# Kernel optimization log

Measured on AMD Instinct MI355X. Metric: run time of the kernel, lower is better.

The kernel has to match this reference:

```python
import jax, jax.numpy as jnp
import numpy as np

B, L, D, H, HD, K = 1, 1024, 1024, 16, 64, 16
EPS = 1e-5

def _l2norm(x):
    n = jnp.sqrt(jnp.sum(x * x, axis=-1, keepdims=True))
    return x / jnp.maximum(n, 1e-12)

def _lin(x, w, b):
    return x @ w.T + b

def _lrelu2(x, alpha=0.01):
    y = jnp.where(x > 0, x, alpha * x)
    return y * y

def _forward(x, spectral_basis, M_phi_w, M_phi_b, wq_w, wq_b, wk_w, wk_b,
             wv_w, wv_b, wo_w, wo_b, wg_z_w, wg_z_b, kv_norm_scale):
    Bx, Lx, Dx = x.shape
    bhld = x.reshape(Bx, Lx, H, HD).transpose(0, 2, 1, 3)          # [B,H,L,h]
    # stu_conv: causal conv of every channel with each of K shared filters (FFT form)
    n = 2 * Lx
    Xf = jnp.fft.rfft(bhld, n=n, axis=2)                            # [B,H,F,h]
    Ff = jnp.fft.rfft(spectral_basis, n=n, axis=0)                  # [F,K]
    conv = jnp.fft.irfft(Xf[:, :, :, None, :] * Ff[None, None, :, :, None], n=n, axis=2)[:, :, :Lx]  # [B,H,L,K,h]
    x_tilde = conv.transpose(0, 2, 3, 1, 4).reshape(Bx, Lx, K * H * HD)
    x_tilde = _lin(x_tilde, M_phi_w, M_phi_b)                       # [B,L,D]
    q = _lin(x_tilde, wq_w, wq_b).reshape(Bx, Lx, H, HD).transpose(0, 2, 1, 3)
    k = _lin(x_tilde, wk_w, wk_b).reshape(Bx, Lx, H, HD).transpose(0, 2, 1, 3)
    v = _lin(x_tilde, wv_w, wv_b).reshape(Bx, Lx, H, HD).transpose(0, 2, 1, 3)
    k = _l2norm(k)
    v = _l2norm(v)
    sim = jnp.einsum('bhld,bhld->bhl', q, k)                        # [B,H,L]
    # Z[b,h,s,p,n] = k[b,h,s,n] * v[b,h,s,p]
    Z = v[..., :, None] * k[..., None, :]                           # [B,H,L,h,h]
    Z = Z * kv_norm_scale
    gates_logits = Z.reshape(Bx, H, Lx, HD * HD) @ wg_z_w.T + wg_z_b  # [B,H,L,1]
    gates_z = (_lrelu2(gates_logits) + EPS)[..., 0]                 # [B,H,L]
    gated_Z = Z * gates_z[..., None, None]
    # online-softmax associative scan over sequence: running (max, norm, exp-weighted v)
    def combine(a, b):
        ma, na, va = a
        mb, nb, vb = b
        m = jnp.maximum(ma, mb)
        ea = jnp.exp(ma - m)
        eb = jnp.exp(mb - m)
        return (m, na * ea + nb * eb, va * ea[..., None] + vb * eb[..., None])
    max_cumul, norm_cumul, v_cumul = jax.lax.associative_scan(
        combine, (sim, jnp.ones_like(sim), v), axis=2)
    Z_cumul = jnp.cumsum(gated_Z, axis=2)
    gate_cumul = jnp.cumsum(gates_z, axis=2)
    linear_attn = v_cumul / (norm_cumul[..., None] + EPS)           # [B,H,L,h]
    weights = jnp.exp(sim - max_cumul) / (norm_cumul + EPS)         # [B,H,L]
    Hm = Z_cumul / (gate_cumul[..., None, None] + EPS)              # [B,H,L,h,h]
    Y_base = jnp.einsum('bhtp,bhtpn->bhtn', q, Hm)                  # [B,H,L,h]
    # torch einsum broadcasts the size-1 p-dim of linear_attn.unsqueeze(-2):
    Y_lin = jnp.sum(q, axis=-1, keepdims=True) * linear_attn        # [B,H,L,h]
    Y = Y_base + (Y_lin - Y_base) * weights[..., None]
    Y = Y.transpose(0, 2, 1, 3).reshape(Bx, Lx, Dx)
    Y = _l2norm(Y)
    return _lin(Y, wo_w, wo_b)

def setup_inputs() -> dict:
    key = jax.random.key(0)
    ks = jax.random.split(key, 16)
    def nrm(k, shape, scale):
        return jax.random.normal(k, shape, dtype=jnp.float32) * scale
    return {
        'x': nrm(ks[0], (B, L, D), 1.0),
        'spectral_basis': nrm(ks[1], (L, K), 1.0 / np.sqrt(L)),
        'M_phi_w': nrm(ks[2], (D, K * H * HD), 1.0 / np.sqrt(K * H * HD)),
        'M_phi_b': jnp.zeros((D,), jnp.float32),
        'wq_w': nrm(ks[3], (D, D), 1.0 / np.sqrt(D)),
        'wq_b': jnp.zeros((D,), jnp.float32),
        'wk_w': nrm(ks[4], (D, D), 1.0 / np.sqrt(D)),
        'wk_b': jnp.zeros((D,), jnp.float32),
        'wv_w': nrm(ks[5], (D, D), 1.0 / np.sqrt(D)),
        'wv_b': jnp.zeros((D,), jnp.float32),
        'wo_w': nrm(ks[6], (D, D), 1.0 / np.sqrt(D)),
        'wo_b': jnp.zeros((D,), jnp.float32),
        'wg_z_w': nrm(ks[7], (1, HD * HD), 1.0 / np.sqrt(HD * HD)),
        'wg_z_b': jnp.zeros((1,), jnp.float32),
        'kv_norm_scale': jnp.ones((1, H, 1, 1, 1), jnp.float32),
    }

def reference(x, spectral_basis, M_phi_w, M_phi_b, wq_w, wq_b, wk_w, wk_b,
              wv_w, wv_b, wo_w, wo_b, wg_z_w, wg_z_b, kv_norm_scale):
    return _forward(x, spectral_basis, M_phi_w, M_phi_b, wq_w, wq_b, wk_w, wk_b,
                    wv_w, wv_b, wo_w, wo_b, wg_z_w, wg_z_b, kv_norm_scale)
```

## Files before the change

### kernel.cpp

```cpp
#include <hip/hip_runtime.h>
#include <hip/hip_bf16.h>

typedef __hip_bfloat16 bf16;
typedef __attribute__((ext_vector_type(8))) short short8;
typedef __attribute__((ext_vector_type(4))) float f32x4;

struct bf16x8 { bf16 v[8]; };
struct bf16x4 { bf16 v[4]; };

__device__ __forceinline__ void gload_lds16(const void* g, void* l) {
  __builtin_amdgcn_global_load_lds(
      (const __attribute__((address_space(1))) void*)g,
      (__attribute__((address_space(3))) void*)l, 16, 0, 0);
}

__device__ __forceinline__ float wave_sum(float x) {
#pragma unroll
  for (int o = 32; o > 0; o >>= 1) x += __shfl_xor(x, o, 64);
  return x;
}

__global__ void prep_cast_k(const float* __restrict__ mphiW,
                            const float* __restrict__ wq, const float* __restrict__ wk,
                            const float* __restrict__ wv, const float* __restrict__ wo,
                            const float* __restrict__ x,
                            const float* __restrict__ bq, const float* __restrict__ bk,
                            const float* __restrict__ bv,
                            const float* __restrict__ basis,
                            bf16* __restrict__ mphi_bf, bf16* __restrict__ wqkv,
                            bf16* __restrict__ wo_bf, bf16* __restrict__ x_bf,
                            float* __restrict__ qkv_bias, bf16* __restrict__ T) {
  int b = blockIdx.x, tid = threadIdx.x;
  if (b >= 10764) {
    size_t i8 = (size_t)(b - 10764) * 256 + tid;
    size_t i = i8 * 8;
    int s0 = (int)(i & 1023);
    int l = (int)((i >> 10) & 1023);
    int k = (int)(i >> 20);
    bf16x8 o;
#pragma unroll
    for (int j = 0; j < 8; j++) {
      int s = s0 + j;
      o.v[j] = (s <= l) ? __float2bfloat16(basis[(size_t)(l - s) * 16 + k])
                        : __float2bfloat16(0.f);
    }
    ((bf16x8*)T)[i8] = o;
    return;
  }
  const float* src; bf16* dst; int i;
  if (b < 8192) { src = mphiW; dst = mphi_bf; i = b * 256 + tid; }
  else if (b < 10240) {
    int bb = b - 8192;
    src = (bb < 512) ? wq : (bb < 1024) ? wk : (bb < 1536) ? wv : wo;
    dst = (bb < 512) ? wqkv : (bb < 1024) ? (wqkv + 1048576)
         : (bb < 1536) ? (wqkv + 2097152) : wo_bf;
    i = (bb & 511) * 256 + tid;
  } else if (b < 10752) { src = x; dst = x_bf; i = (b - 10240) * 256 + tid; }
  else {
    int j = (b - 10752) * 256 + tid;
    if (j < 3072) {
      const float* s = (j < 1024) ? bq : (j < 2048) ? bk : bv;
      qkv_bias[j] = s[j & 1023];
    }
    return;
  }
  const float4* p = (const float4*)src + (size_t)i * 2;
  float4 a = p[0], c = p[1];
  bf16x8 o;
  o.v[0] = __float2bfloat16(a.x); o.v[1] = __float2bfloat16(a.y);
  o.v[2] = __float2bfloat16(a.z); o.v[3] = __float2bfloat16(a.w);
  o.v[4] = __float2bfloat16(c.x); o.v[5] = __float2bfloat16(c.y);
  o.v[6] = __float2bfloat16(c.z); o.v[7] = __float2bfloat16(c.w);
  ((bf16x8*)dst)[i] = o;
}

template<int TRI, int OUTBF, int HASB, int DBUF, int SK3>
__global__ void gemm_bt(const bf16* __restrict__ A, long sAb, int lda,
                        const bf16* __restrict__ B, long sBb, int ldb,
                        void* __restrict__ Cv, void* __restrict__ Cv2, int nbz1,
                        long sCb, int ldc,
                        const float* __restrict__ bias, int sbias, int K) {
  constexpr int NB = DBUF ? 2 : 1;
  __shared__ bf16 As[NB][128 * 64];
  __shared__ bf16 Bs[NB][128 * 64];
  const int tid = threadIdx.x;
  const int lane = tid & 63;
  const int wid = tid >> 6;
  const int wr = wid >> 1, wc = wid & 1;
  const int cpx = gridDim.x >> 3;
  const int logical = (blockIdx.x & 7) * cpx + (blockIdx.x >> 3);
  const int bx = logical & 7, by = (logical >> 3) & 7, bz = logical >> 6;
  const int r0 = by * 128, c0 = bx * 128;
  const bf16* Ab;
  const bf16* Bb;
  if (SK3) {
    int w_ = bz % 3, kh_ = bz / 3;
    Ab = A + kh_ * 512;
    Bb = B + (size_t)w_ * sBb + kh_ * 512;
  } else {
    Ab = A + (size_t)bz * sAb;
    Bb = B + (size_t)bz * sBb;
  }
  f32x4 acc[4][4] = {};
  const int nt = (TRI ? min(K, r0 + 128) : K) >> 6;

  const int srow = tid >> 3, scol = (tid & 7) << 3;

#define STAGE(buf, t)                                                         \
  {                                                                           \
    const int k0_ = (t) << 6;                                                 \
    _Pragma("unroll")                                                         \
    for (int i = 0; i < 4; i++) {                                             \
      int row = i * 32 + srow;                                                \
      gload_lds16(Ab + (size_t)(r0 + row) * lda + k0_ + scol,                 \
                  &As[buf][(row << 6) + scol]);                               \
    }                                                                         \
    _Pragma("unroll")                                                         \
    for (int i = 0; i < 4; i++) {                                             \
      int row = i * 32 + srow;                                                \
      gload_lds16(Bb + (size_t)(c0 + row) * ldb + k0_ + scol,                 \
                  &Bs[buf][(row << 6) + scol]);                               \
    }                                                                         \
  }

  int cur = 0;
  if (DBUF) STAGE(0, 0)
  for (int t = 0; t < nt; ++t) {
    if (DBUF) {
      if (t + 1 < nt) {
        STAGE(cur ^ 1, t + 1)
        asm volatile("s_waitcnt vmcnt(8)" ::: "memory");
      } else {
        asm volatile("s_waitcnt vmcnt(0)" ::: "memory");
      }
      __syncthreads();
    } else {
      __syncthreads();
      STAGE(0, t)
      asm volatile("s_waitcnt vmcnt(0)" ::: "memory");
      __syncthreads();
    }
#pragma unroll
    for (int ks = 0; ks < 2; ks++) {
      const int colo = ks * 32 + (lane >> 4) * 8;
      short8 af[4], bfr[4];
#pragma unroll
      for (int m = 0; m < 4; m++)
        af[m] = *(const short8*)&As[cur][(wr * 64 + m * 16 + (lane & 15)) * 64 + colo];
#pragma unroll
      for (int n = 0; n < 4; n++)
        bfr[n] = *(const short8*)&Bs[cur][(wc * 64 + n * 16 + (lane & 15)) * 64 + colo];
#pragma unroll
      for (int m = 0; m < 4; m++)
#pragma unroll
        for (int n = 0; n < 4; n++)
          acc[m][n] = __builtin_amdgcn_mfma_f32_16x16x32_bf16(af[m], bfr[n], acc[m][n], 0, 0, 0);
    }
    if (DBUF) { __syncthreads(); cur ^= 1; }
  }
#undef STAGE

  void* Cb = (bz < nbz1) ? Cv : Cv2;
  const int bzl = (bz < nbz1) ? bz : bz - nbz1;
  const int rb = r0 + wr * 64 + ((lane >> 4) << 2);
  const int cb = c0 + wc * 64 + (lane & 15);
#pragma unroll
  for (int n = 0; n < 4; n++) {
    const int col = cb + n * 16;
    float bv = HASB ? bias[bz * sbias + col] : 0.f;
#pragma unroll
    for (int m = 0; m < 4; m++) {
#pragma unroll
      for (int j = 0; j < 4; j++) {
        const int row = rb + m * 16 + j;
        size_t off = (size_t)bzl * sCb + (size_t)row * ldc + col;
        float v = acc[m][n][j] + bv;
        if (OUTBF) ((bf16*)Cb)[off] = __float2bfloat16(v);
        else       ((float*)Cb)[off] = v;
      }
    }
  }
}

__global__ void reduce16_k(const float* __restrict__ pA, const float* __restrict__ pB,
                           const float* __restrict__ bias, bf16* __restrict__ out) {
  int i4 = blockIdx.x * 256 + threadIdx.x;
  float4 v = *((const float4*)bias + (i4 & 255));
#pragma unroll
  for (int j = 0; j < 8; j++) {
    float4 a = *((const float4*)pA + i4 + j * 262144);
    v.x += a.x; v.y += a.y; v.z += a.z; v.w += a.w;
  }
#pragma unroll
  for (int j = 0; j < 8; j++) {
    float4 a = *((const float4*)pB + i4 + j * 262144);
    v.x += a.x; v.y += a.y; v.z += a.z; v.w += a.w;
  }
  bf16x4 o;
  o.v[0] = __float2bfloat16(v.x); o.v[1] = __float2bfloat16(v.y);
  o.v[2] = __float2bfloat16(v.z); o.v[3] = __float2bfloat16(v.w);
  ((bf16x4*)out)[i4] = o;
}

__global__ void reduce4f_k(const float* __restrict__ p, const float* __restrict__ bias,
                           float* __restrict__ out) {
  int i4 = blockIdx.x * 256 + threadIdx.x;
  float4 v = *((const float4*)bias + (i4 & 255));
#pragma unroll
  for (int j = 0; j < 4; j++) {
    float4 a = *((const float4*)p + i4 + j * 262144);
    v.x += a.x; v.y += a.y; v.z += a.z; v.w += a.w;
  }
  ((float4*)out)[i4] = v;
}

__global__ void qkv_post_k(const float* __restrict__ qkv, const float* __restrict__ W,
                           const float* __restrict__ wgb, const float* __restrict__ scale,
                           const float* __restrict__ bias,
                           float* __restrict__ kn, float* __restrict__ vn,
                           float* __restrict__ sim, float* __restrict__ gz, float* __restrict__ qs) {
  __shared__ float Wl[64][65];
  int tid = threadIdx.x;
#pragma unroll
  for (int i = 0; i < 16; i++) {
    int c = i * 256 + tid;
    Wl[c >> 6][c & 63] = W[c];
  }
  __syncthreads();
  int lane = tid & 63;
  int gw = blockIdx.x * 4 + (tid >> 6);
  int h = gw >> 10, l = gw & 1023;
  const float* base = qkv + (size_t)l * 1024 + h * 64 + lane;
  float q = base[0] + base[3145728] + bias[h * 64 + lane];
  float k = base[1048576] + base[4194304] + bias[1024 + h * 64 + lane];
  float v = base[2097152] + base[5242880] + bias[2048 + h * 64 + lane];
  float knv = k * (1.f / fmaxf(sqrtf(wave_sum(k * k)), 1e-12f));
  float vnv = v * (1.f / fmaxf(sqrtf(wave_sum(v * v)), 1e-12f));
  float simv = wave_sum(q * knv);
  float qsv = wave_sum(q);
  float inner = 0.f;
#pragma unroll 8
  for (int n = 0; n < 64; n++)
    inner += Wl[lane][n] * __shfl(knv, n, 64);
  float gl = wave_sum(vnv * inner) * scale[h] + wgb[0];
  float yy = gl > 0.f ? gl : 0.01f * gl;
  float gzz = yy * yy + 1e-5f;
  size_t o = ((size_t)h * 1024 + l) * 64 + lane;
  kn[o] = knv; vn[o] = vnv;
  if (lane == 0) {
    sim[h * 1024 + l] = simv; gz[h * 1024 + l] = gzz; qs[h * 1024 + l] = qsv;
  }
}

__global__ void scan_outer_k(const float* __restrict__ sim, const float* __restrict__ gz,
                             const float* __restrict__ vn, const float* __restrict__ kn,
                             float* __restrict__ vloc, float* __restrict__ mloc,
                             float* __restrict__ nloc, float* __restrict__ gloc,
                             float* __restrict__ mA, float* __restrict__ nA,
                             float* __restrict__ vA, float* __restrict__ gA,
                             float* __restrict__ Mc) {
  __shared__ float vns[64][64], kns[64][64], gzs[64];
  int c = blockIdx.x, h = blockIdx.y, tid = threadIdx.x;
  size_t base = ((size_t)h * 1024 + c * 64) * 64;
#pragma unroll
  for (int i = 0; i < 16; i++) {
    int e = i * 256 + tid;
    vns[e >> 6][e & 63] = vn[base + e];
    kns[e >> 6][e & 63] = kn[base + e];
  }
  if (tid < 64) gzs[tid] = gz[h * 1024 + c * 64 + tid];
  __syncthreads();
  float acc[16] = {};
  for (int s = 0; s < 64; s++) {
    float g = gzs[s];
#pragma unroll
    for (int i = 0; i < 16; i++) {
      int pn = i * 256 + tid;
      acc[i] += (g * vns[s][pn >> 6]) * kns[s][pn & 63];
    }
  }
  size_t ob = (size_t)(h * 16 + c) * 4096;
#pragma unroll
  for (int i = 0; i < 16; i++) Mc[ob + i * 256 + tid] = acc[i];
  if (tid < 64) {
    int lane = tid;
    size_t hb = (size_t)h * 1024 + c * 64;
    float m = -1e30f, n = 0.f, v = 0.f, g = 0.f;
    for (int i = 0; i < 64; i++) {
      float s = sim[hb + i];
      float vv = vns[i][lane];
      float mn = fmaxf(m, s);
      float eo = expf(m - mn);
      float en = expf(s - mn);
      n = n * eo + en;
      v = v * eo + en * vv;
      m = mn;
      g += gzs[i];
      vloc[(hb + i) * 64 + lane] = v;
      if (lane == 0) { mloc[hb + i] = m; nloc[hb + i] = n; gloc[hb + i] = g; }
    }
    size_t ix = (size_t)h * 16 + c;
    vA[ix * 64 + lane] = v;
    if (lane == 0) { mA[ix] = m; nA[ix] = n; gA[ix] = g; }
  }
}

__global__ void scan_apply_k(const float* __restrict__ sim,
                             const float* __restrict__ mloc, const float* __restrict__ nloc,
                             const float* __restrict__ gloc, const float* __restrict__ vloc,
                             const float* __restrict__ mA, const float* __restrict__ nA,
                             const float* __restrict__ gA, const float* __restrict__ vA,
                             float* __restrict__ linb, float* __restrict__ wtb,
                             float* __restrict__ gcb) {
  int c = blockIdx.x, h = blockIdx.y;
  int tid = threadIdx.x, lane = tid & 63, w = tid >> 6;
  float m = -1e30f, n = 0.f, v = 0.f, g = 0.f;
  for (int cc = 0; cc < c; cc++) {
    size_t ix = (size_t)h * 16 + cc;
    float mb = mA[ix], nb = nA[ix], gb = gA[ix];
    float vb = vA[ix * 64 + lane];
    float mn = fmaxf(m, mb);
    float ea = expf(m - mn), eb = expf(mb - mn);
    n = n * ea + nb * eb;
    v = v * ea + vb * eb;
    m = mn; g += gb;
  }
#pragma unroll 4
  for (int i = 0; i < 16; i++) {
    int row = w * 16 + i;
    int gw = h * 1024 + c * 64 + row;
    float ml = mloc[gw], nl = nloc[gw], gl = gloc[gw];
    float vl = vloc[(size_t)gw * 64 + lane];
    float mf = fmaxf(m, ml);
    float ep = expf(m - mf), el = expf(ml - mf);
    float nf = n * ep + nl * el;
    float vf = v * ep + vl * el;
    float inv = 1.f / (nf + 1e-5f);
    linb[(size_t)gw * 64 + lane] = vf * inv;
    if (lane == 0) {
      wtb[gw] = expf(sim[gw] - mf) * inv;
      gcb[gw] = g + gl;
    }
  }
}

__launch_bounds__(256)
__global__ void attn_mm_k(const float* __restrict__ qkvf, const float* __restrict__ vn,
                          const float* __restrict__ kn, const float* __restrict__ gz,
                          const float* __restrict__ qs, const float* __restrict__ Mc,
                          const float* __restrict__ wtb, const float* __restrict__ gcb,
                          const float* __restrict__ linb, const float* __restrict__ scale,
                          const float* __restrict__ bias, float* __restrict__ Yc) {
  __shared__ bf16 qs_[64 * 72], vs_[64 * 72], ksT[64 * 72], SsT[64 * 72], Ps[64 * 72];
  __shared__ float gzs[64];
  int c = blockIdx.x, h = blockIdx.y, tid = threadIdx.x;
  int lane = tid & 63, w = tid >> 6;
  size_t base = ((size_t)h * 1024 + c * 64) * 64;
#pragma unroll
  for (int i = 0; i < 16; i++) {
    int e = i * 256 + tid, r = e >> 6, cc = e & 63;
    float qv = qkvf[(size_t)(c * 64 + r) * 1024 + h * 64 + cc]
             + qkvf[(size_t)(c * 64 + r) * 1024 + h * 64 + cc + 3145728]
             + bias[h * 64 + cc];
    qs_[r * 72 + cc] = __float2bfloat16(qv);
    vs_[r * 72 + cc] = __float2bfloat16(vn[base + e]);
    ksT[cc * 72 + r] = __float2bfloat16(kn[base + e]);
  }
  if (tid < 64) gzs[tid] = gz[h * 1024 + c * 64 + tid];
  {
    float4 a0 = {0,0,0,0}, a1 = {0,0,0,0}, a2 = {0,0,0,0}, a3 = {0,0,0,0};
    const float* McH = Mc + (size_t)h * 16 * 4096;
    for (int cc = 0; cc < c; cc++) {
      const float4* p = (const float4*)(McH + cc * 4096) + tid * 4;
      float4 t0 = p[0], t1 = p[1], t2 = p[2], t3 = p[3];
      a0.x += t0.x; a0.y += t0.y; a0.z += t0.z; a0.w += t0.w;
      a1.x += t1.x; a1.y += t1.y; a1.z += t1.z; a1.w += t1.w;
      a2.x += t2.x; a2.y += t2.y; a2.z += t2.z; a2.w += t2.w;
      a3.x += t3.x; a3.y += t3.y; a3.z += t3.z; a3.w += t3.w;
    }
    float4 av[4] = {a0, a1, a2, a3};
#pragma unroll
    for (int j = 0; j < 4; j++) {
      int idx = tid * 4 + j;
      int p = idx >> 4, nb = (idx & 15) * 4;
      SsT[(nb + 0) * 72 + p] = __float2bfloat16(av[j].x);
      SsT[(nb + 1) * 72 + p] = __float2bfloat16(av[j].y);
      SsT[(nb + 2) * 72 + p] = __float2bfloat16(av[j].z);
      SsT[(nb + 3) * 72 + p] = __float2bfloat16(av[j].w);
    }
  }
  __syncthreads();
  const int fr = lane & 15, fq = lane >> 4;
  const int colo0 = fq * 8;
  {
    f32x4 pacc[4] = {};
#pragma unroll
    for (int ks2 = 0; ks2 < 2; ks2++) {
      int colo = ks2 * 32 + colo0;
      short8 a = *(const short8*)&qs_[(w * 16 + fr) * 72 + colo];
#pragma unroll
      for (int st = 0; st < 4; st++) {
        short8 b = *(const short8*)&vs_[(st * 16 + fr) * 72 + colo];
        pacc[st] = __builtin_amdgcn_mfma_f32_16x16x32_bf16(a, b, pacc[st], 0, 0, 0);
      }
    }
#pragma unroll
    for (int st = 0; st < 4; st++) {
      int s = st * 16 + fr;
      float g = gzs[s];
#pragma unroll
      for (int j = 0; j < 4; j++) {
        int t = w * 16 + fq * 4 + j;
        Ps[t * 72 + s] = __float2bfloat16((s <= t) ? pacc[st][j] * g : 0.f);
      }
    }
  }
  __syncthreads();
  f32x4 y[4] = {};
#pragma unroll
  for (int ks2 = 0; ks2 < 2; ks2++) {
    int colo = ks2 * 32 + colo0;
    short8 a  = *(const short8*)&qs_[(w * 16 + fr) * 72 + colo];
    short8 a2 = *(const short8*)&Ps[(w * 16 + fr) * 72 + colo];
#pragma unroll
    for (int nt = 0; nt < 4; nt++) {
      short8 b  = *(const short8*)&SsT[(nt * 16 + fr) * 72 + colo];
      short8 b2 = *(const short8*)&ksT[(nt * 16 + fr) * 72 + colo];
      y[nt] = __builtin_amdgcn_mfma_f32_16x16x32_bf16(a, b, y[nt], 0, 0, 0);
      y[nt] = __builtin_amdgcn_mfma_f32_16x16x32_bf16(a2, b2, y[nt], 0, 0, 0);
    }
  }
  float sc = scale[h];
#pragma unroll
  for (int j = 0; j < 4; j++) {
    int t = w * 16 + fq * 4 + j;
    int l = c * 64 + t;
    size_t il = (size_t)h * 1024 + l;
    float gcv = gcb[il], wv = wtb[il], qv = qs[il];
    float den = 1.f / (gcv + 1e-5f);
#pragma unroll
    for (int nt = 0; nt < 4; nt++) {
      int n = nt * 16 + fr;
      float yb = sc * y[nt][j] * den;
      float yl = qv * linb[il * 64 + n];
      Yc[(size_t)l * 1024 + h * 64 + n] = yb + (yl - yb) * wv;
    }
  }
}

__global__ void rownorm_cast_k(const float* __restrict__ Y, bf16* __restrict__ out) {
  __shared__ float red[4];
  int l = blockIdx.x, tid = threadIdx.x;
  float4 v = ((const float4*)(Y + (size_t)l * 1024))[tid];
  float ss = v.x * v.x + v.y * v.y + v.z * v.z + v.w * v.w;
  ss = wave_sum(ss);
  int wid = tid >> 6, lane = tid & 63;
  if (lane == 0) red[wid] = ss;
  __syncthreads();
  float tot = red[0] + red[1] + red[2] + red[3];
  float inv = 1.f / fmaxf(sqrtf(tot), 1e-12f);
  bf16x4 o;
  o.v[0] = __float2bfloat16(v.x * inv); o.v[1] = __float2bfloat16(v.y * inv);
  o.v[2] = __float2bfloat16(v.z * inv); o.v[3] = __float2bfloat16(v.w * inv);
  ((bf16x4*)(out + (size_t)l * 1024))[tid] = o;
}

extern "C" void kernel_launch(void* const* d_in, const int* in_sizes, int n_in,
                              void* d_out, int out_size, void* d_ws, size_t ws_size,
                              hipStream_t stream) {
  (void)in_sizes; (void)n_in; (void)out_size; (void)ws_size;
  const float* x     = (const float*)d_in[0];
  const float* basis = (const float*)d_in[1];
  const float* mphiW = (const float*)d_in[2];
  const float* mphiB = (const float*)d_in[3];
  const float* wqW = (const float*)d_in[4];  const float* wqB = (const float*)d_in[5];
  const float* wkW = (const float*)d_in[6];  const float* wkB = (const float*)d_in[7];
  const float* wvW = (const float*)d_in[8];  const float* wvB = (const float*)d_in[9];
  const float* woW = (const float*)d_in[10]; const float* woB = (const float*)d_in[11];
  const float* wgW = (const float*)d_in[12]; const float* wgB = (const float*)d_in[13];
  const float* kvs = (const float*)d_in[14];
  float* out = (float*)d_out;
  char* ws = (char*)d_ws;

  bf16*  Y_T     = (bf16*)(ws + 0x0000000UL);
  bf16*  Tbuf    = (bf16*)(ws + 0x2000000UL);
  bf16*  mphi_bf = (bf16*)(ws + 0x4000000UL);
  float* part2a  = (float*)(ws + 0x4000000UL);
  float* qkvf    = (float*)(ws + 0x4000000UL);
  float* part8   = (float*)(ws + 0x4000000UL);
  bf16*  x_bf    = (bf16*)(ws + 0x6000000UL);
  bf16*  xtil_bf = (bf16*)(ws + 0x6200000UL);
  bf16*  wqkv_bf = (bf16*)(ws + 0x6400000UL);
  bf16*  wo_bf   = (bf16*)(ws + 0x6A00000UL);
  float* qkv_bias= (float*)(ws + 0x6C00000UL);
  float* part2b  = (float*)(ws + 0x6C10000UL);
  float* kn      = (float*)(ws + 0x6C10000UL);
  float* vn      = (float*)(ws + 0x7010000UL);
  float* Mc      = (float*)(ws + 0x7410000UL);
  float* Yc      = (float*)(ws + 0x7810000UL);
  bf16*  ynorm   = (bf16*)(ws + 0x7C10000UL);
  float* simb    = (float*)(ws + 0x7E10000UL);
  float* gzb     = (float*)(ws + 0x7E20000UL);
  float* qsb     = (float*)(ws + 0x7E30000UL);
  float* wtb     = (float*)(ws + 0x7E40000UL);
  float* gcb     = (float*)(ws + 0x7E50000UL);
  float* vloc = (float*)(ws + 0x2000000UL);
  float* mloc = (float*)(ws + 0x2400000UL);
  float* nloc = (float*)(ws + 0x2410000UL);
  float* gloc = (float*)(ws + 0x2420000UL);
  float* mA   = (float*)(ws + 0x2430000UL);
  float* nA   = (float*)(ws + 0x2431000UL);
  float* gA   = (float*)(ws + 0x2432000UL);
  float* vA   = (float*)(ws + 0x2440000UL);
  float* linb = (float*)(ws + 0x2500000UL);

  prep_cast_k<<<18956, 256, 0, stream>>>(mphiW, wqW, wkW, wvW, woW, x, wqB, wkB, wvB,
                                         basis, mphi_bf, wqkv_bf, wo_bf, x_bf,
                                         qkv_bias, Tbuf);

  gemm_bt<0, 1, 0, 0, 0><<<1024, 256, 0, stream>>>(
      mphi_bf, 1024L, 16384, x_bf, 0L, 1024, (void*)Y_T, (void*)Y_T, 1 << 28,
      1048576L, 1024, nullptr, 0, 1024);

  gemm_bt<1, 0, 0, 0, 0><<<1024, 256, 0, stream>>>(
      Tbuf, 1048576L, 1024, Y_T, 1048576L, 1024, (void*)part2a, (void*)part2b, 8,
      1048576L, 1024, nullptr, 0, 1024);
  reduce16_k<<<1024, 256, 0, stream>>>(part2a, part2b, mphiB, xtil_bf);

  gemm_bt<0, 0, 0, 1, 1><<<384, 256, 0, stream>>>(
      xtil_bf, 0L, 1024, wqkv_bf, 1048576L, 1024, (void*)qkvf, (void*)qkvf, 1 << 28,
      1048576L, 1024, nullptr, 0, 512);

  qkv_post_k<<<4096, 256, 0, stream>>>(qkvf, wgW, wgB, kvs, qkv_bias,
                                       kn, vn, simb, gzb, qsb);

  scan_outer_k<<<dim3(16, 16), 256, 0, stream>>>(simb, gzb, vn, kn,
                                                 vloc, mloc, nloc, gloc,
                                                 mA, nA, vA, gA, Mc);

  scan_apply_k<<<dim3(16, 16), 256, 0, stream>>>(simb, mloc, nloc, gloc, vloc,
                                                 mA, nA, gA, vA, linb, wtb, gcb);

  attn_mm_k<<<dim3(16, 16), 256, 0, stream>>>(qkvf, vn, kn, gzb, qsb, Mc,
                                              wtb, gcb, linb, kvs, qkv_bias, Yc);

  rownorm_cast_k<<<1024, 256, 0, stream>>>(Yc, ynorm);

  gemm_bt<0, 0, 0, 1, 0><<<256, 256, 0, stream>>>(
      ynorm, 256L, 1024, wo_bf, 256L, 1024, (void*)part8, (void*)part8, 1 << 28,
      1048576L, 1024, nullptr, 0, 256);
  reduce4f_k<<<1024, 256, 0, stream>>>(part8, woB, out);
}
```

Baseline: 234.1 us.

## Generate Toeplitz conv operand on the fly instead of materializing it

Drops the explicit 16x1024x1024 bf16 Toeplitz matrix that prep_cast_k used to build in memory. A new GEMM kernel instead builds A-fragments directly from a per-filter transposed basis held in LDS, and a small kernel transposes and casts the basis up front. This removes about 32MB of writes plus the matching reads by the GEMM. The cost is scalar LDS gathers with branches when building each fragment, which may slow the inner MFMA loop.

```diff
diff --git a/kernel.cpp b/kernel.cpp
--- a/kernel.cpp
+++ b/kernel.cpp
@@ -18,6 +18,12 @@
 #pragma unroll
   for (int o = 32; o > 0; o >>= 1) x += __shfl_xor(x, o, 64);
   return x;
+}
+
+__global__ void transpose_basis_k(const float* __restrict__ basis,
+                                  bf16* __restrict__ basisT_bf) {
+  int idx = blockIdx.x * 256 + threadIdx.x;
+  basisT_bf[(idx & 15) * 1024 + (idx >> 4)] = __float2bfloat16(basis[idx]);
 }
 
 __global__ void prep_cast_k(const float* __restrict__ mphiW,
@@ -26,27 +32,10 @@
                             const float* __restrict__ x,
                             const float* __restrict__ bq, const float* __restrict__ bk,
                             const float* __restrict__ bv,
-                            const float* __restrict__ basis,
                             bf16* __restrict__ mphi_bf, bf16* __restrict__ wqkv,
                             bf16* __restrict__ wo_bf, bf16* __restrict__ x_bf,
-                            float* __restrict__ qkv_bias, bf16* __restrict__ T) {
+                            float* __restrict__ qkv_bias) {
   int b = blockIdx.x, tid = threadIdx.x;
-  if (b >= 10764) {
-    size_t i8 = (size_t)(b - 10764) * 256 + tid;
-    size_t i = i8 * 8;
-    int s0 = (int)(i & 1023);
-    int l = (int)((i >> 10) & 1023);
-    int k = (int)(i >> 20);
-    bf16x8 o;
-#pragma unroll
-    for (int j = 0; j < 8; j++) {
-      int s = s0 + j;
-      o.v[j] = (s <= l) ? __float2bfloat16(basis[(size_t)(l - s) * 16 + k])
-                        : __float2bfloat16(0.f);
-    }
-    ((bf16x8*)T)[i8] = o;
-    return;
-  }
   const float* src; bf16* dst; int i;
   if (b < 8192) { src = mphiW; dst = mphi_bf; i = b * 256 + tid; }
   else if (b < 10240) {
@@ -182,6 +171,85 @@
   }
 }
 
+__launch_bounds__(256)
+__global__ void gemm_toep_k(const bf16* __restrict__ bTall, const bf16* __restrict__ B,
+                            long sBb, int ldb, float* __restrict__ Cv,
+                            float* __restrict__ Cv2, int nbz1, long sCb, int ldc,
+                            int K) {
+  __shared__ bf16 Bs[128 * 64];
+  __shared__ uint2 bTu[256];
+  unsigned short* bT = (unsigned short*)bTu;
+  const int tid = threadIdx.x;
+  const int lane = tid & 63;
+  const int wid = tid >> 6;
+  const int wr = wid >> 1, wc = wid & 1;
+  const int cpx = gridDim.x >> 3;
+  const int logical = (blockIdx.x & 7) * cpx + (blockIdx.x >> 3);
+  const int bx = logical & 7, by = (logical >> 3) & 7, bz = logical >> 6;
+  const int r0 = by * 128, c0 = bx * 128;
+  bTu[tid] = ((const uint2*)(bTall + (size_t)bz * 1024))[tid];
+  const bf16* Bb = B + (size_t)bz * sBb;
+  f32x4 acc[4][4] = {};
+  const int nt = min(K, r0 + 128) >> 6;
+  const int srow = tid >> 3, scol = (tid & 7) << 3;
+  const int fr = lane & 15, fq = lane >> 4;
+
+  for (int t = 0; t < nt; ++t) {
+    __syncthreads();
+    const int k0 = t << 6;
+#pragma unroll
+    for (int i = 0; i < 4; i++) {
+      int row = i * 32 + srow;
+      gload_lds16(Bb + (size_t)(c0 + row) * ldb + k0 + scol, &Bs[(row << 6) + scol]);
+    }
+    asm volatile("s_waitcnt vmcnt(0)" ::: "memory");
+    __syncthreads();
+#pragma unroll
+    for (int ks = 0; ks < 2; ks++) {
+      const int colo = ks * 32 + fq * 8;
+      const int gcol = k0 + colo;
+      short8 af[4], bfr[4];
+#pragma unroll
+      for (int m = 0; m < 4; m++) {
+        int grow = r0 + wr * 64 + m * 16 + fr;
+        int d0 = grow - gcol;
+#pragma unroll
+        for (int j = 0; j < 8; j++) {
+          int d = d0 - j;
+          int dc = d < 0 ? 0 : d;
+          unsigned short v = bT[dc];
+          af[m][j] = (short)(d >= 0 ? v : 0);
+        }
+      }
+#pragma unroll
+      for (int n = 0; n < 4; n++)
+        bfr[n] = *(const short8*)&Bs[(wc * 64 + n * 16 + fr) * 64 + colo];
+#pragma unroll
+      for (int m = 0; m < 4; m++)
+#pragma unroll
+        for (int n = 0; n < 4; n++)
+          acc[m][n] = __builtin_amdgcn_mfma_f32_16x16x32_bf16(af[m], bfr[n], acc[m][n], 0, 0, 0);
+    }
+  }
+
+  float* Cb = (bz < nbz1) ? Cv : Cv2;
+  const int bzl = (bz < nbz1) ? bz : bz - nbz1;
+  const int rb = r0 + wr * 64 + (fq << 2);
+  const int cb = c0 + wc * 64 + fr;
+#pragma unroll
+  for (int n = 0; n < 4; n++) {
+    const int col = cb + n * 16;
+#pragma unroll
+    for (int m = 0; m < 4; m++) {
+#pragma unroll
+      for (int j = 0; j < 4; j++) {
+        const int row = rb + m * 16 + j;
+        Cb[(size_t)bzl * sCb + (size_t)row * ldc + col] = acc[m][n][j];
+      }
+    }
+  }
+}
+
 __global__ void reduce16_k(const float* __restrict__ pA, const float* __restrict__ pB,
                            const float* __restrict__ bias, bf16* __restrict__ out) {
   int i4 = blockIdx.x * 256 + threadIdx.x;
@@ -483,7 +551,6 @@
   char* ws = (char*)d_ws;
 
   bf16*  Y_T     = (bf16*)(ws + 0x0000000UL);
-  bf16*  Tbuf    = (bf16*)(ws + 0x2000000UL);
   bf16*  mphi_bf = (bf16*)(ws + 0x4000000UL);
   float* part2a  = (float*)(ws + 0x4000000UL);
   float* qkvf    = (float*)(ws + 0x4000000UL);
@@ -513,18 +580,18 @@
   float* gA   = (float*)(ws + 0x2432000UL);
   float* vA   = (float*)(ws + 0x2440000UL);
   float* linb = (float*)(ws + 0x2500000UL);
-
-  prep_cast_k<<<18956, 256, 0, stream>>>(mphiW, wqW, wkW, wvW, woW, x, wqB, wkB, wvB,
-                                         basis, mphi_bf, wqkv_bf, wo_bf, x_bf,
-                                         qkv_bias, Tbuf);
+  bf16*  basisT_bf = (bf16*)(ws + 0x3000000UL);
+
+  transpose_basis_k<<<64, 256, 0, stream>>>(basis, basisT_bf);
+  prep_cast_k<<<10764, 256, 0, stream>>>(mphiW, wqW, wkW, wvW, woW, x, wqB, wkB, wvB,
+                                         mphi_bf, wqkv_bf, wo_bf, x_bf, qkv_bias);
 
   gemm_bt<0, 1, 0, 0, 0><<<1024, 256, 0, stream>>>(
       mphi_bf, 1024L, 16384, x_bf, 0L, 1024, (void*)Y_T, (void*)Y_T, 1 << 28,
       1048576L, 1024, nullptr, 0, 1024);
 
-  gemm_bt<1, 0, 0, 0, 0><<<1024, 256, 0, stream>>>(
-      Tbuf, 1048576L, 1024, Y_T, 1048576L, 1024, (void*)part2a, (void*)part2b, 8,
-      1048576L, 1024, nullptr, 0, 1024);
+  gemm_toep_k<<<1024, 256, 0, stream>>>(
+      basisT_bf, Y_T, 1048576L, 1024, part2a, part2b, 8, 1048576L, 1024, 1024);
   reduce16_k<<<1024, 256, 0, stream>>>(part2a, part2b, mphiB, xtil_bf);
 
   gemm_bt<0, 0, 0, 1, 1><<<384, 256, 0, stream>>>(
```

After: 242.7 us. 1.04x slower.
